# Performance work log

Measured on AMD Instinct MI355X. Metric: run time of the kernel, lower is better.

The kernel has to match this reference:

```python
import jax, jax.numpy as jnp
import numpy as np

N_FFT = 1024
HOP = 256
WIN = 1024
PAD = (WIN - HOP) // 2  # 'same' padding trim
B, NBINS, T = 32, N_FFT // 2 + 1, 2048


def setup_inputs() -> dict:
    key = jax.random.key(0)
    k1, k2 = jax.random.split(key)
    spec_real = jax.random.normal(k1, (B, NBINS, T), dtype=jnp.float32)
    spec_imag = jax.random.normal(k2, (B, NBINS, T), dtype=jnp.float32)
    # Hann window, as used by neural vocoders (periodic hann)
    n = jnp.arange(WIN, dtype=jnp.float32)
    window = 0.5 - 0.5 * jnp.cos(2.0 * jnp.pi * n / WIN)
    return {"spec_real": spec_real, "spec_imag": spec_imag, "window": window}


def reference(spec_real, spec_imag, window):
    spec = jax.lax.complex(spec_real, spec_imag)            # (B, N, T)
    ifft = jnp.fft.irfft(spec, n=N_FFT, axis=1, norm="backward")  # (B, n_fft, T)
    ifft = ifft * window[None, :, None]                     # windowed frames
    b, _, t = spec_real.shape
    out_size = (t - 1) * HOP + WIN
    idx = jnp.arange(t)[None, :] * HOP + jnp.arange(WIN)[:, None]
    y = jnp.zeros((b, out_size), dtype=ifft.dtype).at[:, idx].add(ifft)
    env = jnp.zeros((out_size,), dtype=window.dtype).at[idx].add(
        jnp.broadcast_to(jnp.square(window)[:, None], (WIN, t))
    )
    return y[:, PAD:-PAD] / env[PAD:-PAD]
```

## Files before the change

kernel.cpp:

```cpp
#include <hip/hip_runtime.h>
#include <hip/hip_fp16.h>

#define NBINS 513
#define TFR   2048
#define NB    32
#define WIN   1024
#define HOP   256
#define PADT  384
#define OPB   524288
#define FR    16
#define TILES (TFR / FR)
#define SPAN  (FR * HOP)
#define FSTRIDE 545
#define PIDX(i) ((i) + ((i) >> 4))
#define C45 0.70710678118654752f
#define TWOPI_1024 0.0061359231515425649f
#define SSC   (1.0f / 512.0f * 2.0f / 3.0f)
#define CDLT  0.99998117528260114f
#define SDLT  0.00613588464915448f

__device__ __forceinline__ float2 cadd(float2 a, float2 b){ return make_float2(a.x+b.x, a.y+b.y); }
__device__ __forceinline__ float2 csub(float2 a, float2 b){ return make_float2(a.x-b.x, a.y-b.y); }
__device__ __forceinline__ float2 cmul(float2 a, float2 b){ return make_float2(a.x*b.x - a.y*b.y, a.x*b.y + a.y*b.x); }
__device__ __forceinline__ float2 h2f(__half2 h){ return __half22float2(h); }
__device__ __forceinline__ __half2 f2h(float x, float y){ return __floats2half2_rn(x, y); }

__device__ __forceinline__ void wavesync() {
    __builtin_amdgcn_wave_barrier();
    asm volatile("" ::: "memory");
}

#define BFLY8(u0,u1,u2,u3,u4,u5,u6,u7, v0,v1,v2,v3,v4,v5,v6,v7)            \
    float2 s0=cadd(u0,u4), t0=csub(u0,u4);                                  \
    float2 s1=cadd(u1,u5), t1=csub(u1,u5);                                  \
    float2 s2=cadd(u2,u6), t2=csub(u2,u6);                                  \
    float2 s3=cadd(u3,u7), t3=csub(u3,u7);                                  \
    t1 = make_float2(C45*(t1.x - t1.y),  C45*(t1.x + t1.y));                \
    t2 = make_float2(-t2.y, t2.x);                                          \
    t3 = make_float2(-C45*(t3.x + t3.y), C45*(t3.x - t3.y));                \
    float2 p0=cadd(s0,s2), p2=csub(s0,s2);                                  \
    float2 p1=cadd(s1,s3), p3=csub(s1,s3); p3 = make_float2(-p3.y, p3.x);   \
    float2 q0=cadd(t0,t2), q2=csub(t0,t2);                                  \
    float2 q1=cadd(t1,t3), q3=csub(t1,t3); q3 = make_float2(-q3.y, q3.x);   \
    float2 v0=cadd(p0,p1), v4=csub(p0,p1);                                  \
    float2 v2=cadd(p2,p3), v6=csub(p2,p3);                                  \
    float2 v1=cadd(q0,q1), v5=csub(q0,q1);                                  \
    float2 v3=cadd(q2,q3), v7=csub(q2,q3);

template<int L>
__device__ __forceinline__ void fft_stage(__half2* __restrict__ row,
                                          const float2* __restrict__ ph, int i)
{
    const int k    = i & (L - 1);
    const int base = ((i & ~(L - 1)) << 3) + k;
    float2 u0 = h2f(row[PIDX(base + 0*L)]);
    float2 u1 = h2f(row[PIDX(base + 1*L)]);
    float2 u2 = h2f(row[PIDX(base + 2*L)]);
    float2 u3 = h2f(row[PIDX(base + 3*L)]);
    float2 u4 = h2f(row[PIDX(base + 4*L)]);
    float2 u5 = h2f(row[PIDX(base + 5*L)]);
    float2 u6 = h2f(row[PIDX(base + 6*L)]);
    float2 u7 = h2f(row[PIDX(base + 7*L)]);
    BFLY8(u0,u1,u2,u3,u4,u5,u6,u7, v0,v1,v2,v3,v4,v5,v6,v7)
    if constexpr (L > 1) {
        const float2 w1 = ph[k * (128 / L)];
        float2 wq = w1;
        v1 = cmul(v1, wq);
        wq = cmul(wq, w1); v2 = cmul(v2, wq);
        wq = cmul(wq, w1); v3 = cmul(v3, wq);
        wq = cmul(wq, w1); v4 = cmul(v4, wq);
        wq = cmul(wq, w1); v5 = cmul(v5, wq);
        wq = cmul(wq, w1); v6 = cmul(v6, wq);
        wq = cmul(wq, w1); v7 = cmul(v7, wq);
    }
    row[PIDX(base + 0*L)] = f2h(v0.x, v0.y);
    row[PIDX(base + 1*L)] = f2h(v1.x, v1.y);
    row[PIDX(base + 2*L)] = f2h(v2.x, v2.y);
    row[PIDX(base + 3*L)] = f2h(v3.x, v3.y);
    row[PIDX(base + 4*L)] = f2h(v4.x, v4.y);
    row[PIDX(base + 5*L)] = f2h(v5.x, v5.y);
    row[PIDX(base + 6*L)] = f2h(v6.x, v6.y);
    row[PIDX(base + 7*L)] = f2h(v7.x, v7.y);
}

__device__ __forceinline__ float2 hann_pair(const float2* __restrict__ ph, int n)
{
    const bool mir = n > 256;
    const int  m   = mir ? 512 - n : n;
    const float2 cs = ph[m];
    const float c = mir ? -cs.x : cs.x;
    const float s = cs.y;
    const float w0 = 1.0f - c*c;
    const float c2 = 2.0f*c*c - 1.0f;
    const float s2 = 2.0f*c*s;
    const float w1 = 0.5f - 0.5f*(c2*CDLT - s2*SDLT);
    return make_float2(w0, w1);
}

__global__ __launch_bounds__(256) void zero_seams(float* __restrict__ out)
{
    const int total = NB * (TILES + 1) * 768;
    for (int id = blockIdx.x * 256 + threadIdx.x; id < total; id += gridDim.x * 256) {
        const int q = id % 768;
        const int r = id / 768;
        const int s = r % (TILES + 1);
        const int bb = r / (TILES + 1);
        const int p  = s * SPAN + q;
        const int oi = p - PADT;
        if ((unsigned)oi < (unsigned)OPB) out[(size_t)bb * OPB + oi] = 0.f;
    }
}

__global__ __launch_bounds__(256, 4) void istft16(
    const float* __restrict__ sr, const float* __restrict__ si,
    float* __restrict__ out)
{
    __shared__ __half2 stile[FR * FSTRIDE];
    __shared__ float2  ph[257];

    const int tid = threadIdx.x;
    const int bid = blockIdx.x;
    const int nwg = NB * TILES;
    const int swz = (bid & 7) * (nwg >> 3) + (bid >> 3);
    const int b    = swz / TILES;
    const int tile = swz % TILES;
    const int j0   = tile * FR;

    const size_t gbase = (size_t)b * NBINS * TFR + (size_t)j0;
    const size_t gaA = gbase + (size_t)tid * TFR;
    const size_t gaB = gbase + (size_t)(512 - tid) * TFR;
    float4 rA0 = *(const float4*)(sr + gaA);
    float4 rA1 = *(const float4*)(sr + gaA + 4);
    float4 rA2 = *(const float4*)(sr + gaA + 8);
    float4 rA3 = *(const float4*)(sr + gaA + 12);
    float4 iA0 = *(const float4*)(si + gaA);
    float4 iA1 = *(const float4*)(si + gaA + 4);
    float4 iA2 = *(const float4*)(si + gaA + 8);
    float4 iA3 = *(const float4*)(si + gaA + 12);
    float4 rB0 = *(const float4*)(sr + gaB);
    float4 rB1 = *(const float4*)(sr + gaB + 4);
    float4 rB2 = *(const float4*)(sr + gaB + 8);
    float4 rB3 = *(const float4*)(sr + gaB + 12);
    float4 iB0 = *(const float4*)(si + gaB);
    float4 iB1 = *(const float4*)(si + gaB + 4);
    float4 iB2 = *(const float4*)(si + gaB + 8);
    float4 iB3 = *(const float4*)(si + gaB + 12);

    float2 rc, ic;
    if (tid < 8) {
        const size_t gaC = gbase + (size_t)256 * TFR + 2*tid;
        rc = *(const float2*)(sr + gaC);
        ic = *(const float2*)(si + gaC);
    }
    if (tid == 0) {
        const float4 z4 = make_float4(0.f,0.f,0.f,0.f);
        iA0=iA1=iA2=iA3=z4; iB0=iB1=iB2=iB3=z4;
    }

    for (int m = tid; m < 257; m += 256) {
        float sv, cv;
        sincosf(TWOPI_1024 * (float)m, &sv, &cv);
        ph[m] = make_float2(cv, sv);
    }

    {
        const float h = 0.5f * SSC;
        float swt, cwt;
        sincosf(TWOPI_1024 * (float)tid, &swt, &cwt);
        const int pk  = PIDX(tid);
        const int pk2 = PIDX(512 - tid);
#define TRICK(F, XKX, XKY, XMX, XMY) do {                                   \
            const float Ex = h*((XKX)+(XMX)), Ey = h*((XKY)-(XMY));         \
            const float Dx = h*((XKX)-(XMX)), Dy = h*((XKY)+(XMY));         \
            const float Ox = Dx*cwt - Dy*swt, Oy = Dx*swt + Dy*cwt;         \
            stile[(F)*FSTRIDE + pk]  = f2h(Ex - Oy, Ey + Ox);               \
            stile[(F)*FSTRIDE + pk2] = f2h(Ex + Oy, Ox - Ey);               \
        } while (0)
        TRICK(0,  rA0.x, iA0.x, rB0.x, iB0.x);
        TRICK(1,  rA0.y, iA0.y, rB0.y, iB0.y);
        TRICK(2,  rA0.z, iA0.z, rB0.z, iB0.z);
        TRICK(3,  rA0.w, iA0.w, rB0.w, iB0.w);
        TRICK(4,  rA1.x, iA1.x, rB1.x, iB1.x);
        TRICK(5,  rA1.y, iA1.y, rB1.y, iB1.y);
        TRICK(6,  rA1.z, iA1.z, rB1.z, iB1.z);
        TRICK(7,  rA1.w, iA1.w, rB1.w, iB1.w);
        TRICK(8,  rA2.x, iA2.x, rB2.x, iB2.x);
        TRICK(9,  rA2.y, iA2.y, rB2.y, iB2.y);
        TRICK(10, rA2.z, iA2.z, rB2.z, iB2.z);
        TRICK(11, rA2.w, iA2.w, rB2.w, iB2.w);
        TRICK(12, rA3.x, iA3.x, rB3.x, iB3.x);
        TRICK(13, rA3.y, iA3.y, rB3.y, iB3.y);
        TRICK(14, rA3.z, iA3.z, rB3.z, iB3.z);
        TRICK(15, rA3.w, iA3.w, rB3.w, iB3.w);
#undef TRICK
        if (tid < 8) {
            stile[(2*tid)  *FSTRIDE + PIDX(256)] = f2h(rc.x * SSC, -ic.x * SSC);
            stile[(2*tid+1)*FSTRIDE + PIDX(256)] = f2h(rc.y * SSC, -ic.y * SSC);
        }
    }
    __syncthreads();

    {
        const int f  = tid >> 4;
        __half2* row = &stile[f * FSTRIDE];
        const int i0 = tid & 15;
        fft_stage<64>(row, ph, i0);
        fft_stage<64>(row, ph, i0 + 16);
        fft_stage<64>(row, ph, i0 + 32);
        fft_stage<64>(row, ph, i0 + 48);
        wavesync();
        fft_stage<8>(row, ph, i0);
        fft_stage<8>(row, ph, i0 + 16);
        fft_stage<8>(row, ph, i0 + 32);
        fft_stage<8>(row, ph, i0 + 48);
        wavesync();
        fft_stage<1>(row, ph, i0);
        fft_stage<1>(row, ph, i0 + 16);
        fft_stage<1>(row, ph, i0 + 32);
        fft_stage<1>(row, ph, i0 + 48);
        __syncthreads();
    }

    const int nE = tid;
    const int nO = (tid + 128) & 255;
    const float2 wE0 = hann_pair(ph, nE);
    const float2 wE1 = hann_pair(ph, nE + 256);
    const float2 wO0 = hann_pair(ph, nO);
    const float2 wO1 = hann_pair(ph, nO + 256);

    float2 a0 = make_float2(0.f,0.f), a1=a0, a2=a0, a3=a0, a4=a0,
           a5 = a0, a6=a0, a7=a0, a8=a0, a9=a0;
    const bool tlo = (tid < 128);

#define OLA_STEP(F, KK, ACCV, W) do {                                       \
        const int n_ = (((F) & 1) ? nO : nE) + ((KK) << 8);                 \
        const int j_ = ((n_ & 7) << 6) | (n_ & 56) | (n_ >> 6);             \
        const float2 z_ = h2f(stile[(F)*FSTRIDE + PIDX(j_)]);               \
        ACCV.x += z_.x * W.x;                                               \
        ACCV.y += z_.y * W.y;                                               \
    } while (0)

    OLA_STEP(0,0,a0,wE0);  OLA_STEP(0,1,a1,wE1);
    if (tlo) { OLA_STEP(1,0,a1,wO0);  OLA_STEP(1,1,a2,wO1); }
    else     { OLA_STEP(1,0,a0,wO0);  OLA_STEP(1,1,a1,wO1); }
    OLA_STEP(2,0,a1,wE0);  OLA_STEP(2,1,a2,wE1);
    if (tlo) { OLA_STEP(3,0,a2,wO0);  OLA_STEP(3,1,a3,wO1); }
    else     { OLA_STEP(3,0,a1,wO0);  OLA_STEP(3,1,a2,wO1); }
    OLA_STEP(4,0,a2,wE0);  OLA_STEP(4,1,a3,wE1);
    if (tlo) { OLA_STEP(5,0,a3,wO0);  OLA_STEP(5,1,a4,wO1); }
    else     { OLA_STEP(5,0,a2,wO0);  OLA_STEP(5,1,a3,wO1); }
    OLA_STEP(6,0,a3,wE0);  OLA_STEP(6,1,a4,wE1);
    if (tlo) { OLA_STEP(7,0,a4,wO0);  OLA_STEP(7,1,a5,wO1); }
    else     { OLA_STEP(7,0,a3,wO0);  OLA_STEP(7,1,a4,wO1); }
    OLA_STEP(8,0,a4,wE0);  OLA_STEP(8,1,a5,wE1);
    if (tlo) { OLA_STEP(9,0,a5,wO0);  OLA_STEP(9,1,a6,wO1); }
    else     { OLA_STEP(9,0,a4,wO0);  OLA_STEP(9,1,a5,wO1); }
    OLA_STEP(10,0,a5,wE0); OLA_STEP(10,1,a6,wE1);
    if (tlo) { OLA_STEP(11,0,a6,wO0); OLA_STEP(11,1,a7,wO1); }
    else     { OLA_STEP(11,0,a5,wO0); OLA_STEP(11,1,a6,wO1); }
    OLA_STEP(12,0,a6,wE0); OLA_STEP(12,1,a7,wE1);
    if (tlo) { OLA_STEP(13,0,a7,wO0); OLA_STEP(13,1,a8,wO1); }
    else     { OLA_STEP(13,0,a6,wO0); OLA_STEP(13,1,a7,wO1); }
    OLA_STEP(14,0,a7,wE0); OLA_STEP(14,1,a8,wE1);
    if (tlo) { OLA_STEP(15,0,a8,wO0); OLA_STEP(15,1,a9,wO1); }
    else     { OLA_STEP(15,0,a7,wO0); OLA_STEP(15,1,a8,wO1); }
#undef OLA_STEP

    const size_t ob = (size_t)b * OPB;
    const int pb = tile * SPAN;
#define STORE_SEAM(A, G) do {                                               \
        const int oi_ = pb + 2*(tid + 256*(G)) - PADT;                      \
        if ((unsigned)oi_ < (unsigned)OPB)       atomicAdd(&out[ob + oi_],     A.x); \
        if ((unsigned)(oi_+1) < (unsigned)OPB)   atomicAdd(&out[ob + oi_ + 1], A.y); \
    } while (0)
#define STORE_PLAIN(A, G) do {                                              \
        const int oi_ = pb + 2*(tid + 256*(G)) - PADT;                      \
        *(float2*)(out + ob + oi_) = A;                                     \
    } while (0)

    STORE_SEAM(a0, 0);
    if (tlo) STORE_SEAM(a1, 1);
    else     STORE_PLAIN(a1, 1);
    STORE_PLAIN(a2, 2);
    STORE_PLAIN(a3, 3);
    STORE_PLAIN(a4, 4);
    STORE_PLAIN(a5, 5);
    STORE_PLAIN(a6, 6);
    STORE_PLAIN(a7, 7);
    STORE_SEAM(a8, 8);
    if (tlo) STORE_SEAM(a9, 9);
#undef STORE_SEAM
#undef STORE_PLAIN
}

__global__ __launch_bounds__(256) void edge_fix(float* __restrict__ out)
{
    const int id = blockIdx.x * 256 + threadIdx.x;
    if (id >= 768 * NB) return;
    const int bb = id / 768;
    const int r  = id % 768;
    const int oi = (r < 384) ? r : (OPB - 768 + r);
    const int p  = oi + PADT;
    int jlo = (p - 768) >> 8; if (jlo < 0) jlo = 0;
    int jhi = p >> 8;         if (jhi > TFR - 1) jhi = TFR - 1;
    float e = 0.f;
    for (int j = jlo; j <= jhi; ++j) {
        const float wv = 0.5f - 0.5f * cosf(TWOPI_1024 * (float)(p - j * HOP));
        e += wv * wv;
    }
    out[(size_t)bb * OPB + oi] *= 1.5f / e;
}

extern "C" void kernel_launch(void* const* d_in, const int* in_sizes, int n_in,
                              void* d_out, int out_size, void* d_ws, size_t ws_size,
                              hipStream_t stream) {
    const float* sr = (const float*)d_in[0];
    const float* si = (const float*)d_in[1];
    float* out = (float*)d_out;

    hipLaunchKernelGGL(zero_seams, dim3(2048), dim3(256), 0, stream, out);
    hipLaunchKernelGGL(istft16, dim3(NB * TILES), dim3(256), 0, stream, sr, si, out);
    hipLaunchKernelGGL(edge_fix, dim3((768 * NB + 255) / 256), dim3(256), 0, stream, out);
}
```

Baseline: 119.2 us.

## Replace three radix-8 LDS passes with register-resident 32x16 FFT decomposition

Swaps the 512-point complex FFT, previously three radix-8 passes that each went through shared memory, for a two-pass 32x16 decomposition. Each thread does a 32-point FFT in registers with on-the-fly twiddles, then a 16-point FFT over contiguous vectorised float4 LDS loads. The shared twiddle/phase table is dropped: twiddles come from constants and per-thread sincos, and the Hann weights are derived algebraically from the thread's own cos/sin. The new padded layout (stride 20 per 16 entries) is meant to avoid bank conflicts, at the cost of more shared memory per block and higher register pressure from 32-element register arrays, which may reduce occupancy.

New measurement: 130.5 us. 1.09x slower.

```diff
diff --git a/kernel.cpp b/kernel.cpp
--- a/kernel.cpp
+++ b/kernel.cpp
@@ -11,10 +11,11 @@
 #define FR    16
 #define TILES (TFR / FR)
 #define SPAN  (FR * HOP)
-#define FSTRIDE 545
-#define PIDX(i) ((i) + ((i) >> 4))
+#define FSTRIDE 636
+#define PHI(s) ((s) + 4*((s) >> 4))
 #define C45 0.70710678118654752f
 #define TWOPI_1024 0.0061359231515425649f
+#define TWOPI_512  0.0122718463030851306f
 #define SSC   (1.0f / 512.0f * 2.0f / 3.0f)
 #define CDLT  0.99998117528260114f
 #define SDLT  0.00613588464915448f
@@ -30,66 +31,37 @@
     asm volatile("" ::: "memory");
 }
 
-#define BFLY8(u0,u1,u2,u3,u4,u5,u6,u7, v0,v1,v2,v3,v4,v5,v6,v7)            \
-    float2 s0=cadd(u0,u4), t0=csub(u0,u4);                                  \
-    float2 s1=cadd(u1,u5), t1=csub(u1,u5);                                  \
-    float2 s2=cadd(u2,u6), t2=csub(u2,u6);                                  \
-    float2 s3=cadd(u3,u7), t3=csub(u3,u7);                                  \
-    t1 = make_float2(C45*(t1.x - t1.y),  C45*(t1.x + t1.y));                \
-    t2 = make_float2(-t2.y, t2.x);                                          \
-    t3 = make_float2(-C45*(t3.x + t3.y), C45*(t3.x - t3.y));                \
-    float2 p0=cadd(s0,s2), p2=csub(s0,s2);                                  \
-    float2 p1=cadd(s1,s3), p3=csub(s1,s3); p3 = make_float2(-p3.y, p3.x);   \
-    float2 q0=cadd(t0,t2), q2=csub(t0,t2);                                  \
-    float2 q1=cadd(t1,t3), q3=csub(t1,t3); q3 = make_float2(-q3.y, q3.x);   \
-    float2 v0=cadd(p0,p1), v4=csub(p0,p1);                                  \
-    float2 v2=cadd(p2,p3), v6=csub(p2,p3);                                  \
-    float2 v1=cadd(q0,q1), v5=csub(q0,q1);                                  \
-    float2 v3=cadd(q2,q3), v7=csub(q2,q3);
-
-template<int L>
-__device__ __forceinline__ void fft_stage(__half2* __restrict__ row,
-                                          const float2* __restrict__ ph, int i)
+__device__ __forceinline__ float2 twid(int j) {
+    const float C[17] = { 1.f, 0.98078528f, 0.92387953f, 0.83146961f, 0.70710678f,
+                          0.55557023f, 0.38268343f, 0.19509032f, 0.f, -0.19509032f,
+                         -0.38268343f, -0.55557023f, -0.70710678f, -0.83146961f,
+                         -0.92387953f, -0.98078528f, -1.f };
+    const int js = (j <= 8) ? (8 - j) : (j - 8);
+    return make_float2(C[j], C[js]);
+}
+
+template<int N>
+__device__ __forceinline__ void ifft_reg(float2* v) {
+    if constexpr (N == 1) {
+        (void)v;
+    } else {
+        float2 e[N/2], o[N/2];
+        #pragma unroll
+        for (int i = 0; i < N/2; ++i) { e[i] = v[2*i]; o[i] = v[2*i+1]; }
+        ifft_reg<N/2>(e);
+        ifft_reg<N/2>(o);
+        #pragma unroll
+        for (int q = 0; q < N/2; ++q) {
+            const float2 w = twid(q * (32 / N));
+            const float2 t = cmul(o[q], w);
+            v[q]       = cadd(e[q], t);
+            v[q + N/2] = csub(e[q], t);
+        }
+    }
+}
+
+__device__ __forceinline__ float2 hann_cs(float c, float s)
 {
-    const int k    = i & (L - 1);
-    const int base = ((i & ~(L - 1)) << 3) + k;
-    float2 u0 = h2f(row[PIDX(base + 0*L)]);
-    float2 u1 = h2f(row[PIDX(base + 1*L)]);
-    float2 u2 = h2f(row[PIDX(base + 2*L)]);
-    float2 u3 = h2f(row[PIDX(base + 3*L)]);
-    float2 u4 = h2f(row[PIDX(base + 4*L)]);
-    float2 u5 = h2f(row[PIDX(base + 5*L)]);
-    float2 u6 = h2f(row[PIDX(base + 6*L)]);
-    float2 u7 = h2f(row[PIDX(base + 7*L)]);
-    BFLY8(u0,u1,u2,u3,u4,u5,u6,u7, v0,v1,v2,v3,v4,v5,v6,v7)
-    if constexpr (L > 1) {
-        const float2 w1 = ph[k * (128 / L)];
-        float2 wq = w1;
-        v1 = cmul(v1, wq);
-        wq = cmul(wq, w1); v2 = cmul(v2, wq);
-        wq = cmul(wq, w1); v3 = cmul(v3, wq);
-        wq = cmul(wq, w1); v4 = cmul(v4, wq);
-        wq = cmul(wq, w1); v5 = cmul(v5, wq);
-        wq = cmul(wq, w1); v6 = cmul(v6, wq);
-        wq = cmul(wq, w1); v7 = cmul(v7, wq);
-    }
-    row[PIDX(base + 0*L)] = f2h(v0.x, v0.y);
-    row[PIDX(base + 1*L)] = f2h(v1.x, v1.y);
-    row[PIDX(base + 2*L)] = f2h(v2.x, v2.y);
-    row[PIDX(base + 3*L)] = f2h(v3.x, v3.y);
-    row[PIDX(base + 4*L)] = f2h(v4.x, v4.y);
-    row[PIDX(base + 5*L)] = f2h(v5.x, v5.y);
-    row[PIDX(base + 6*L)] = f2h(v6.x, v6.y);
-    row[PIDX(base + 7*L)] = f2h(v7.x, v7.y);
-}
-
-__device__ __forceinline__ float2 hann_pair(const float2* __restrict__ ph, int n)
-{
-    const bool mir = n > 256;
-    const int  m   = mir ? 512 - n : n;
-    const float2 cs = ph[m];
-    const float c = mir ? -cs.x : cs.x;
-    const float s = cs.y;
     const float w0 = 1.0f - c*c;
     const float c2 = 2.0f*c*c - 1.0f;
     const float s2 = 2.0f*c*s;
@@ -115,8 +87,7 @@
     const float* __restrict__ sr, const float* __restrict__ si,
     float* __restrict__ out)
 {
-    __shared__ __half2 stile[FR * FSTRIDE];
-    __shared__ float2  ph[257];
+    __shared__ __align__(16) __half2 stile[FR * FSTRIDE];
 
     const int tid = threadIdx.x;
     const int bid = blockIdx.x;
@@ -157,24 +128,19 @@
         iA0=iA1=iA2=iA3=z4; iB0=iB1=iB2=iB3=z4;
     }
 
-    for (int m = tid; m < 257; m += 256) {
-        float sv, cv;
-        sincosf(TWOPI_1024 * (float)m, &sv, &cv);
-        ph[m] = make_float2(cv, sv);
-    }
-
+    float swt, cwt;
+    sincosf(TWOPI_1024 * (float)tid, &swt, &cwt);
     {
         const float h = 0.5f * SSC;
-        float swt, cwt;
-        sincosf(TWOPI_1024 * (float)tid, &swt, &cwt);
-        const int pk  = PIDX(tid);
-        const int pk2 = PIDX(512 - tid);
+        const int pk  = PHI(tid);
+        const int pk2 = PHI(512 - tid);
+        const bool wr2 = (tid != 0);
 #define TRICK(F, XKX, XKY, XMX, XMY) do {                                   \
             const float Ex = h*((XKX)+(XMX)), Ey = h*((XKY)-(XMY));         \
             const float Dx = h*((XKX)-(XMX)), Dy = h*((XKY)+(XMY));         \
             const float Ox = Dx*cwt - Dy*swt, Oy = Dx*swt + Dy*cwt;         \
-            stile[(F)*FSTRIDE + pk]  = f2h(Ex - Oy, Ey + Ox);               \
-            stile[(F)*FSTRIDE + pk2] = f2h(Ex + Oy, Ox - Ey);               \
+            stile[(F)*FSTRIDE + pk] = f2h(Ex - Oy, Ey + Ox);                \
+            if (wr2) stile[(F)*FSTRIDE + pk2] = f2h(Ex + Oy, Ox - Ey);      \
         } while (0)
         TRICK(0,  rA0.x, iA0.x, rB0.x, iB0.x);
         TRICK(1,  rA0.y, iA0.y, rB0.y, iB0.y);
@@ -194,76 +160,109 @@
         TRICK(15, rA3.w, iA3.w, rB3.w, iB3.w);
 #undef TRICK
         if (tid < 8) {
-            stile[(2*tid)  *FSTRIDE + PIDX(256)] = f2h(rc.x * SSC, -ic.x * SSC);
-            stile[(2*tid+1)*FSTRIDE + PIDX(256)] = f2h(rc.y * SSC, -ic.y * SSC);
+            stile[(2*tid)  *FSTRIDE + PHI(256)] = f2h(rc.x * SSC, -ic.x * SSC);
+            stile[(2*tid+1)*FSTRIDE + PHI(256)] = f2h(rc.y * SSC, -ic.y * SSC);
         }
     }
     __syncthreads();
 
     {
-        const int f  = tid >> 4;
-        __half2* row = &stile[f * FSTRIDE];
-        const int i0 = tid & 15;
-        fft_stage<64>(row, ph, i0);
-        fft_stage<64>(row, ph, i0 + 16);
-        fft_stage<64>(row, ph, i0 + 32);
-        fft_stage<64>(row, ph, i0 + 48);
+        const int lw = tid & 63, w = tid >> 6;
+        const int fr = (w << 2) | (lw & 3);
+        const int i0 = lw >> 2;
+        __half2* row = &stile[fr * FSTRIDE];
+
+        {
+            float2 v[32];
+            #pragma unroll
+            for (int p = 0; p < 32; ++p) v[p] = h2f(row[20*p + i0]);
+            ifft_reg<32>(v);
+            float sw1, cw1;
+            sincosf(TWOPI_512 * (float)i0, &sw1, &cw1);
+            const float2 w1 = make_float2(cw1, sw1);
+            float2 wacc = w1;
+            #pragma unroll
+            for (int q = 1; q < 32; ++q) {
+                v[q] = cmul(v[q], wacc);
+                wacc = cmul(wacc, w1);
+            }
+            #pragma unroll
+            for (int q = 0; q < 32; ++q) row[20*q + i0] = f2h(v[q].x, v[q].y);
+        }
         wavesync();
-        fft_stage<8>(row, ph, i0);
-        fft_stage<8>(row, ph, i0 + 16);
-        fft_stage<8>(row, ph, i0 + 32);
-        fft_stage<8>(row, ph, i0 + 48);
-        wavesync();
-        fft_stage<1>(row, ph, i0);
-        fft_stage<1>(row, ph, i0 + 16);
-        fft_stage<1>(row, ph, i0 + 32);
-        fft_stage<1>(row, ph, i0 + 48);
-        __syncthreads();
-    }
-
-    const int nE = tid;
-    const int nO = (tid + 128) & 255;
-    const float2 wE0 = hann_pair(ph, nE);
-    const float2 wE1 = hann_pair(ph, nE + 256);
-    const float2 wO0 = hann_pair(ph, nO);
-    const float2 wO1 = hann_pair(ph, nO + 256);
+
+        #pragma unroll
+        for (int hh = 0; hh < 2; ++hh) {
+            const int qp = i0 + 16*hh;
+            float2 z[16];
+            #pragma unroll
+            for (int c = 0; c < 4; ++c) {
+                const float4 raw = *(const float4*)&row[20*qp + 4*c];
+                const __half2* hp = (const __half2*)&raw;
+                z[4*c+0] = h2f(hp[0]); z[4*c+1] = h2f(hp[1]);
+                z[4*c+2] = h2f(hp[2]); z[4*c+3] = h2f(hp[3]);
+            }
+            ifft_reg<16>(z);
+            #pragma unroll
+            for (int c = 0; c < 4; ++c) {
+                float4 raw;
+                __half2* hp = (__half2*)&raw;
+                hp[0] = f2h(z[4*c+0].x, z[4*c+0].y);
+                hp[1] = f2h(z[4*c+1].x, z[4*c+1].y);
+                hp[2] = f2h(z[4*c+2].x, z[4*c+2].y);
+                hp[3] = f2h(z[4*c+3].x, z[4*c+3].y);
+                *(float4*)&row[20*qp + 4*c] = raw;
+            }
+        }
+    }
+    __syncthreads();
+
+    const bool tlo = (tid < 128);
+    const float c4 = (cwt - swt) * C45, s4 = (cwt + swt) * C45;
+    const float cm = (cwt + swt) * C45, sm = (swt - cwt) * C45;
+    const float2 wE0 = hann_cs(cwt, swt);
+    const float2 wE1 = hann_cs(-swt, cwt);
+    const float2 wO0 = tlo ? hann_cs(c4, s4)  : hann_cs(cm, sm);
+    const float2 wO1 = tlo ? hann_cs(-cm, c4) : hann_cs(c4, s4);
+
+    const int jsE0 = 20*(tid & 31) + (tid >> 5);
+    const int jsE1 = jsE0 + 8;
+    const int jsO0 = 20*(tid & 31) + ((tid >> 5) ^ 4);
+    const int jsO1 = jsO0 + 8;
 
     float2 a0 = make_float2(0.f,0.f), a1=a0, a2=a0, a3=a0, a4=a0,
            a5 = a0, a6=a0, a7=a0, a8=a0, a9=a0;
-    const bool tlo = (tid < 128);
-
-#define OLA_STEP(F, KK, ACCV, W) do {                                       \
-        const int n_ = (((F) & 1) ? nO : nE) + ((KK) << 8);                 \
-        const int j_ = ((n_ & 7) << 6) | (n_ & 56) | (n_ >> 6);             \
-        const float2 z_ = h2f(stile[(F)*FSTRIDE + PIDX(j_)]);               \
+
+#define OLA_STEP(F, JS, ACCV, W) do {                                       \
+        const float2 z_ = h2f(stile[(F)*FSTRIDE + (JS)]);                   \
         ACCV.x += z_.x * W.x;                                               \
         ACCV.y += z_.y * W.y;                                               \
     } while (0)
 
-    OLA_STEP(0,0,a0,wE0);  OLA_STEP(0,1,a1,wE1);
-    if (tlo) { OLA_STEP(1,0,a1,wO0);  OLA_STEP(1,1,a2,wO1); }
-    else     { OLA_STEP(1,0,a0,wO0);  OLA_STEP(1,1,a1,wO1); }
-    OLA_STEP(2,0,a1,wE0);  OLA_STEP(2,1,a2,wE1);
-    if (tlo) { OLA_STEP(3,0,a2,wO0);  OLA_STEP(3,1,a3,wO1); }
-    else     { OLA_STEP(3,0,a1,wO0);  OLA_STEP(3,1,a2,wO1); }
-    OLA_STEP(4,0,a2,wE0);  OLA_STEP(4,1,a3,wE1);
-    if (tlo) { OLA_STEP(5,0,a3,wO0);  OLA_STEP(5,1,a4,wO1); }
-    else     { OLA_STEP(5,0,a2,wO0);  OLA_STEP(5,1,a3,wO1); }
-    OLA_STEP(6,0,a3,wE0);  OLA_STEP(6,1,a4,wE1);
-    if (tlo) { OLA_STEP(7,0,a4,wO0);  OLA_STEP(7,1,a5,wO1); }
-    else     { OLA_STEP(7,0,a3,wO0);  OLA_STEP(7,1,a4,wO1); }
-    OLA_STEP(8,0,a4,wE0);  OLA_STEP(8,1,a5,wE1);
-    if (tlo) { OLA_STEP(9,0,a5,wO0);  OLA_STEP(9,1,a6,wO1); }
-    else     { OLA_STEP(9,0,a4,wO0);  OLA_STEP(9,1,a5,wO1); }
-    OLA_STEP(10,0,a5,wE0); OLA_STEP(10,1,a6,wE1);
-    if (tlo) { OLA_STEP(11,0,a6,wO0); OLA_STEP(11,1,a7,wO1); }
-    else     { OLA_STEP(11,0,a5,wO0); OLA_STEP(11,1,a6,wO1); }
-    OLA_STEP(12,0,a6,wE0); OLA_STEP(12,1,a7,wE1);
-    if (tlo) { OLA_STEP(13,0,a7,wO0); OLA_STEP(13,1,a8,wO1); }
-    else     { OLA_STEP(13,0,a6,wO0); OLA_STEP(13,1,a7,wO1); }
-    OLA_STEP(14,0,a7,wE0); OLA_STEP(14,1,a8,wE1);
-    if (tlo) { OLA_STEP(15,0,a8,wO0); OLA_STEP(15,1,a9,wO1); }
-    else     { OLA_STEP(15,0,a7,wO0); OLA_STEP(15,1,a8,wO1); }
+    OLA_STEP(0,jsE0,a0,wE0);  OLA_STEP(0,jsE1,a1,wE1);
+    if (tlo) { OLA_STEP(1,jsO0,a1,wO0);  OLA_STEP(1,jsO1,a2,wO1); }
+    else     { OLA_STEP(1,jsO0,a0,wO0);  OLA_STEP(1,jsO1,a1,wO1); }
+    OLA_STEP(2,jsE0,a1,wE0);  OLA_STEP(2,jsE1,a2,wE1);
+    if (tlo) { OLA_STEP(3,jsO0,a2,wO0);  OLA_STEP(3,jsO1,a3,wO1); }
+    else     { OLA_STEP(3,jsO0,a1,wO0);  OLA_STEP(3,jsO1,a2,wO1); }
+    OLA_STEP(4,jsE0,a2,wE0);  OLA_STEP(4,jsE1,a3,wE1);
+    if (tlo) { OLA_STEP(5,jsO0,a3,wO0);  OLA_STEP(5,jsO1,a4,wO1); }
+    else     { OLA_STEP(5,jsO0,a2,wO0);  OLA_STEP(5,jsO1,a3,wO1); }
+    OLA_STEP(6,jsE0,a3,wE0);  OLA_STEP(6,jsE1,a4,wE1);
+    if (tlo) { OLA_STEP(7,jsO0,a4,wO0);  OLA_STEP(7,jsO1,a5,wO1); }
+    else     { OLA_STEP(7,jsO0,a3,wO0);  OLA_STEP(7,jsO1,a4,wO1); }
+    OLA_STEP(8,jsE0,a4,wE0);  OLA_STEP(8,jsE1,a5,wE1);
+    if (tlo) { OLA_STEP(9,jsO0,a5,wO0);  OLA_STEP(9,jsO1,a6,wO1); }
+    else     { OLA_STEP(9,jsO0,a4,wO0);  OLA_STEP(9,jsO1,a5,wO1); }
+    OLA_STEP(10,jsE0,a5,wE0); OLA_STEP(10,jsE1,a6,wE1);
+    if (tlo) { OLA_STEP(11,jsO0,a6,wO0); OLA_STEP(11,jsO1,a7,wO1); }
+    else     { OLA_STEP(11,jsO0,a5,wO0); OLA_STEP(11,jsO1,a6,wO1); }
+    OLA_STEP(12,jsE0,a6,wE0); OLA_STEP(12,jsE1,a7,wE1);
+    if (tlo) { OLA_STEP(13,jsO0,a7,wO0); OLA_STEP(13,jsO1,a8,wO1); }
+    else     { OLA_STEP(13,jsO0,a6,wO0); OLA_STEP(13,jsO1,a7,wO1); }
+    OLA_STEP(14,jsE0,a7,wE0); OLA_STEP(14,jsE1,a8,wE1);
+    if (tlo) { OLA_STEP(15,jsO0,a8,wO0); OLA_STEP(15,jsO1,a9,wO1); }
+    else     { OLA_STEP(15,jsO0,a7,wO0); OLA_STEP(15,jsO1,a8,wO1); }
 #undef OLA_STEP
 
     const size_t ob = (size_t)b * OPB;
```
